# Kernel optimization log

Measured on AMD Instinct MI355X. Metric: run time of the kernel, lower is better.

## Reference

```python
import jax, jax.numpy as jnp
import numpy as np

N, E, F, H, C, L, B = 10000, 160000, 128, 8, 64, 8, 64
D = H * C  # 512 = hidden_dim * num_heads
BN_EPS = 1e-5


def setup_inputs() -> dict:
    key = jax.random.key(0)
    ks = jax.random.split(key, 24)

    def w(k, fi, fo, *lead):
        return jax.random.normal(k, (*lead, fi, fo), jnp.float32) / np.sqrt(fi).astype(np.float32)

    inp = {
        "x": jax.random.normal(ks[0], (N, F), jnp.float32),
        "edge_index": jax.random.randint(ks[1], (2, E), 0, N, jnp.int32),
        "batch": jnp.sort(jax.random.randint(ks[2], (N,), 0, B, jnp.int32)),
        # layer 0 projections (F -> D)
        "W0_q": w(ks[3], F, D), "b0_q": jnp.zeros((D,), jnp.float32),
        "W0_k": w(ks[4], F, D), "b0_k": jnp.zeros((D,), jnp.float32),
        "W0_v": w(ks[5], F, D), "b0_v": jnp.zeros((D,), jnp.float32),
        "W0_s": w(ks[6], F, D), "b0_s": jnp.zeros((D,), jnp.float32),
        # layers 1..7 projections (D -> D), stacked
        "Wq": w(ks[7], D, D, L - 1), "bq": jnp.zeros((L - 1, D), jnp.float32),
        "Wk": w(ks[8], D, D, L - 1), "bk": jnp.zeros((L - 1, D), jnp.float32),
        "Wv": w(ks[9], D, D, L - 1), "bv": jnp.zeros((L - 1, D), jnp.float32),
        "Ws": w(ks[10], D, D, L - 1), "bs": jnp.zeros((L - 1, D), jnp.float32),
        # BatchNorm affine params per layer
        "gamma": jnp.ones((L, D), jnp.float32),
        "beta": jnp.zeros((L, D), jnp.float32),
    }
    return inp


def _layer(x, src, dst, Wq, bq, Wk, bk, Wv, bv, Ws, bs, g, b):
    # TransformerConv (concat=True, root_weight=True, beta=False), eval dropout
    n = x.shape[0]
    q = (x @ Wq + bq).reshape(n, H, C)
    k = (x @ Wk + bk).reshape(n, H, C)
    v = (x @ Wv + bv).reshape(n, H, C)
    # per-edge attention logits [E, H]
    a = jnp.einsum('ehc,ehc->eh', q[dst], k[src]) / np.float32(np.sqrt(C))
    # softmax over incoming edges of each destination node
    amax = jax.ops.segment_max(a, dst, num_segments=n)
    a = jnp.exp(a - amax[dst])
    denom = jax.ops.segment_sum(a, dst, num_segments=n)
    a = a / (denom[dst] + 1e-16)
    msg = v[src] * a[:, :, None]                      # [E, H, C]
    out = jax.ops.segment_sum(msg, dst, num_segments=n).reshape(n, D)
    out = out + x @ Ws + bs                           # root/skip connection
    # BatchNorm1d (batch statistics) + ReLU
    mu = out.mean(axis=0)
    var = out.var(axis=0)
    out = (out - mu) / jnp.sqrt(var + BN_EPS) * g + b
    return jax.nn.relu(out)


def reference(x, edge_index, batch, W0_q, b0_q, W0_k, b0_k, W0_v, b0_v, W0_s, b0_s,
              Wq, bq, Wk, bk, Wv, bv, Ws, bs, gamma, beta):
    src, dst = edge_index[0], edge_index[1]
    counts = jnp.maximum(
        jax.ops.segment_sum(jnp.ones((N,), jnp.float32), batch, num_segments=B), 1.0)

    def pool(h):  # global_mean_pool
        return jax.ops.segment_sum(h, batch, num_segments=B) / counts[:, None]

    pooled = []
    h = _layer(x, src, dst, W0_q, b0_q, W0_k, b0_k, W0_v, b0_v, W0_s, b0_s,
               gamma[0], beta[0])
    pooled.append(pool(h))
    for i in range(L - 1):
        h = _layer(h, src, dst, Wq[i], bq[i], Wk[i], bk[i], Wv[i], bv[i],
                   Ws[i], bs[i], gamma[i + 1], beta[i + 1])
        pooled.append(pool(h))
    return jnp.concatenate(pooled, axis=1)  # [B, L*D]
```

## Files before the change

kernel.cpp:

```cpp
#include <hip/hip_runtime.h>

#define NN 10000
#define EE 160000
#define FF 128
#define LL 8
#define BB 64
#define DD 512
#define ND (NN * DD)

typedef unsigned short u16;
typedef __attribute__((ext_vector_type(8))) short short8;
typedef __attribute__((ext_vector_type(8))) _Float16 f16x8;
typedef __attribute__((ext_vector_type(4))) float f32x4;
typedef __attribute__((ext_vector_type(4))) u16 u16x4;

__device__ __forceinline__ u16 f2h(float f) {
  return __builtin_bit_cast(u16, (_Float16)f);
}
__device__ __forceinline__ float h2f(u16 h) {
  return (float)__builtin_bit_cast(_Float16, h);
}

#define GLOAD_LDS16(gp, lp)                                                   \
  __builtin_amdgcn_global_load_lds(                                           \
      (const __attribute__((address_space(1))) void*)(gp),                    \
      (__attribute__((address_space(3))) void*)(lp), 16, 0, 0)

__global__ void k_toh(const float* __restrict__ in, u16* __restrict__ out, int n4) {
  int i = blockIdx.x * 256 + threadIdx.x;
  if (i >= n4) return;
  float4 v = ((const float4*)in)[i];
  u16x4 h;
  h.x = f2h(v.x); h.y = f2h(v.y); h.z = f2h(v.z); h.w = f2h(v.w);
  ((u16x4*)out)[i] = h;
}

__global__ void k_convw(const float* __restrict__ W0, const float* __restrict__ W1,
                        const float* __restrict__ W2, const float* __restrict__ W3,
                        int K, u16* __restrict__ out) {
  __shared__ float t[32][33];
  int z = blockIdx.z;
  int lay = z >> 2, mat = z & 3;
  const float* W = ((mat == 0) ? W0 : (mat == 1) ? W1 : (mat == 2) ? W2 : W3) +
                   (size_t)lay * K * 512;
  int n0 = blockIdx.x * 32, k0 = blockIdx.y * 32;
  int tx = threadIdx.x, ty = threadIdx.y;
#pragma unroll
  for (int i = 0; i < 4; ++i)
    t[ty + 8 * i][tx] = W[(size_t)(k0 + ty + 8 * i) * 512 + n0 + tx];
  __syncthreads();
#pragma unroll
  for (int i = 0; i < 4; ++i) {
    int n = n0 + ty + 8 * i;
    float val = t[tx][ty + 8 * i];
    size_t o = ((size_t)lay * 2048 + mat * 512 + n) * K + k0 + tx;
    out[o] = f2h(val);
  }
}

__global__ void k_fbias(const float* __restrict__ b0q, const float* __restrict__ b0k,
                        const float* __restrict__ b0v, const float* __restrict__ b0s,
                        const float* __restrict__ bq, const float* __restrict__ bk,
                        const float* __restrict__ bv, const float* __restrict__ bs,
                        float* __restrict__ biasf) {
  int j = blockIdx.x * 256 + threadIdx.x;
  int l = j >> 11, m = (j >> 9) & 3, c = j & 511;
  const float* p;
  if (l == 0) {
    p = (m == 0) ? b0q : (m == 1) ? b0k : (m == 2) ? b0v : b0s;
  } else {
    const float* base = (m == 0) ? bq : (m == 1) ? bk : (m == 2) ? bv : bs;
    p = base + (size_t)(l - 1) * 512;
  }
  biasf[j] = p[c];
}

__global__ __launch_bounds__(256) void k_gemm(
    const u16* __restrict__ Ag, const u16* __restrict__ Bg,
    const float* __restrict__ biasf,
    u16* __restrict__ oq16, u16* __restrict__ ok16, u16* __restrict__ ov16,
    float* __restrict__ os, int M, int K) {
  __shared__ short8 sA[2][512], sB[2][512];
  const int tid = threadIdx.x;
  const int jt = blockIdx.x, mt = blockIdx.y;
  const int m0 = mt * 128;
  const int mat = jt >> 2;
  const int nbase = (jt & 3) * 128;
  const int K8 = K >> 3;
  const int l = tid & 63;
  const int wr = tid >> 7, wc = (tid >> 6) & 1;
  const int g = l >> 4, li = l & 15;

  const int c0 = tid, c1 = tid + 256;
  const int r0 = c0 >> 2, r1 = c1 >> 2;
  const int j0 = (c0 & 3) ^ (r0 & 3) ^ ((r0 >> 2) & 3);
  const int j1 = (c1 & 3) ^ (r1 & 3) ^ ((r1 >> 2) & 3);
  const int am0 = min(m0 + r0, M - 1), am1 = min(m0 + r1, M - 1);
  const int brow = mat * 512 + nbase;
  const short8* gA = (const short8*)Ag;
  const short8* gB = (const short8*)Bg;
  const size_t a0 = (size_t)am0 * K8 + j0, a1 = (size_t)am1 * K8 + j1;
  const size_t b0 = (size_t)(brow + r0) * K8 + j0, b1 = (size_t)(brow + r1) * K8 + j1;

  const f32x4 zero4 = {0.f, 0.f, 0.f, 0.f};
  f32x4 acc[4][4];
#pragma unroll
  for (int i = 0; i < 4; ++i)
#pragma unroll
    for (int j = 0; j < 4; ++j) acc[i][j] = zero4;

  auto stage = [&](int buf, int kg) {
    GLOAD_LDS16(gA + a0 + kg, &sA[buf][c0]);
    GLOAD_LDS16(gA + a1 + kg, &sA[buf][c1]);
    GLOAD_LDS16(gB + b0 + kg, &sB[buf][c0]);
    GLOAD_LDS16(gB + b1 + kg, &sB[buf][c1]);
  };

  auto compute = [&](int buf) {
    f16x8 fa[4], fb[4];
#pragma unroll
    for (int mi = 0; mi < 4; ++mi) {
      int row = wr * 64 + mi * 16 + li;
      int idx = row * 4 + (g ^ (row & 3) ^ ((row >> 2) & 3));
      fa[mi] = __builtin_bit_cast(f16x8, sA[buf][idx]);
    }
#pragma unroll
    for (int ni = 0; ni < 4; ++ni) {
      int row = wc * 64 + ni * 16 + li;
      int idx = row * 4 + (g ^ (row & 3) ^ ((row >> 2) & 3));
      fb[ni] = __builtin_bit_cast(f16x8, sB[buf][idx]);
    }
#pragma unroll
    for (int mi = 0; mi < 4; ++mi)
#pragma unroll
      for (int ni = 0; ni < 4; ++ni)
        acc[mi][ni] = __builtin_amdgcn_mfma_f32_16x16x32_f16(fa[mi], fb[ni], acc[mi][ni], 0, 0, 0);
  };

  int buf = 0;
  stage(0, 0);
  __syncthreads();
  for (int kg = 4; kg < K8; kg += 4) {
    stage(buf ^ 1, kg);
    compute(buf);
    __syncthreads();
    buf ^= 1;
  }
  compute(buf);

#pragma unroll
  for (int mi = 0; mi < 4; ++mi) {
    int rbase = m0 + wr * 64 + mi * 16 + g * 4;
#pragma unroll
    for (int ni = 0; ni < 4; ++ni) {
      int col = nbase + wc * 64 + ni * 16 + li;
      float bv = biasf[(jt << 7) + wc * 64 + ni * 16 + li];
#pragma unroll
      for (int r = 0; r < 4; ++r) {
        int gm = rbase + r;
        if (gm < M) {
          float val = acc[mi][ni][r] + bv;
          size_t o = (size_t)gm * 512 + col;
          if (mat == 0) oq16[o] = f2h(val);
          else if (mat == 1) ok16[o] = f2h(val);
          else if (mat == 2) ov16[o] = f2h(val);
          else os[o] = val;
        }
      }
    }
  }
}

__global__ void k_count(const int* __restrict__ dst, int* __restrict__ counts) {
  int e = blockIdx.x * 256 + threadIdx.x;
  if (e < EE) atomicAdd(&counts[dst[e]], 1);
}

__global__ void k_scan(const int* __restrict__ counts, int* __restrict__ offs) {
  __shared__ int ws[1024];
  int t = threadIdx.x;
  int base = t * 10;
  int loc[10];
  int run = 0;
#pragma unroll
  for (int j = 0; j < 10; ++j) {
    int i = base + j;
    int v = (i < NN) ? counts[i] : 0;
    run += v;
    loc[j] = run;
  }
  ws[t] = run;
  __syncthreads();
  for (int d = 1; d < 1024; d <<= 1) {
    int x = (t >= d) ? ws[t - d] : 0;
    __syncthreads();
    ws[t] += x;
    __syncthreads();
  }
  int pre = (t > 0) ? ws[t - 1] : 0;
#pragma unroll
  for (int j = 0; j < 10; ++j) {
    int i = base + j;
    if (i < NN) offs[i + 1] = pre + loc[j];
  }
  if (t == 0) offs[0] = 0;
}

__global__ void k_scatter(const int* __restrict__ src, const int* __restrict__ dst,
                          const int* __restrict__ offs, int* __restrict__ cursor,
                          int* __restrict__ esrc) {
  int e = blockIdx.x * 256 + threadIdx.x;
  if (e < EE) {
    int d = dst[e];
    int pos = offs[d] + atomicAdd(&cursor[d], 1);
    esrc[pos] = src[e];
  }
}

__global__ void k_bstart(const int* __restrict__ batch, int* __restrict__ bstart) {
  int n = blockIdx.x * 256 + threadIdx.x;
  if (n > NN) return;
  if (n == 0) {
    for (int b = 0; b <= batch[0]; ++b) bstart[b] = 0;
  } else if (n == NN) {
    for (int b = batch[NN - 1] + 1; b <= BB; ++b) bstart[b] = NN;
  } else {
    int bp = batch[n - 1], bn = batch[n];
    for (int b = bp + 1; b <= bn; ++b) bstart[b] = n;
  }
}

__device__ __forceinline__ void h8tof(short8 x, float* f) {
  f16x8 h = __builtin_bit_cast(f16x8, x);
#pragma unroll
  for (int j = 0; j < 8; ++j) f[j] = (float)h[j];
}

__global__ __launch_bounds__(256) void k_attn(
    const u16* __restrict__ q16, const u16* __restrict__ k16,
    const u16* __restrict__ v16, float* __restrict__ s,
    const int* __restrict__ offs, const int* __restrict__ esrc) {
  int node = blockIdx.x * 4 + (threadIdx.x >> 6);
  int l = threadIdx.x & 63;
  const short8* qp = (const short8*)q16;
  float qf[8];
  h8tof(qp[(size_t)node * 64 + l], qf);
  const short8* kp = (const short8*)k16;
  const short8* vp = (const short8*)v16;
  float m = -3.4e38f, ssum = 0.f;
  float a[8] = {0.f, 0.f, 0.f, 0.f, 0.f, 0.f, 0.f, 0.f};
  int e0 = offs[node], e1 = offs[node + 1];
  int e = e0;
  for (; e + 2 <= e1; e += 2) {
    int sn0 = esrc[e], sn1 = esrc[e + 1];
    short8 kk0 = kp[(size_t)sn0 * 64 + l];
    short8 kk1 = kp[(size_t)sn1 * 64 + l];
    short8 vv0 = vp[(size_t)sn0 * 64 + l];
    short8 vv1 = vp[(size_t)sn1 * 64 + l];
    float kf0[8], kf1[8];
    h8tof(kk0, kf0);
    h8tof(kk1, kf1);
    float d0 = 0.f, d1 = 0.f;
#pragma unroll
    for (int j = 0; j < 8; ++j) { d0 += qf[j] * kf0[j]; d1 += qf[j] * kf1[j]; }
    d0 += __shfl_xor(d0, 1); d1 += __shfl_xor(d1, 1);
    d0 += __shfl_xor(d0, 2); d1 += __shfl_xor(d1, 2);
    d0 += __shfl_xor(d0, 4); d1 += __shfl_xor(d1, 4);
    float vf0[8], vf1[8];
    h8tof(vv0, vf0);
    h8tof(vv1, vf1);
    {
      float logit = d0 * 0.125f;
      float mn = fmaxf(m, logit);
      float sc = __expf(m - mn), p = __expf(logit - mn);
      ssum = ssum * sc + p;
#pragma unroll
      for (int j = 0; j < 8; ++j) a[j] = a[j] * sc + p * vf0[j];
      m = mn;
    }
    {
      float logit = d1 * 0.125f;
      float mn = fmaxf(m, logit);
      float sc = __expf(m - mn), p = __expf(logit - mn);
      ssum = ssum * sc + p;
#pragma unroll
      for (int j = 0; j < 8; ++j) a[j] = a[j] * sc + p * vf1[j];
      m = mn;
    }
  }
  if (e < e1) {
    int sn0 = esrc[e];
    short8 kk0 = kp[(size_t)sn0 * 64 + l];
    short8 vv0 = vp[(size_t)sn0 * 64 + l];
    float kf0[8], vf0[8];
    h8tof(kk0, kf0);
    h8tof(vv0, vf0);
    float d0 = 0.f;
#pragma unroll
    for (int j = 0; j < 8; ++j) d0 += qf[j] * kf0[j];
    d0 += __shfl_xor(d0, 1);
    d0 += __shfl_xor(d0, 2);
    d0 += __shfl_xor(d0, 4);
    float logit = d0 * 0.125f;
    float mn = fmaxf(m, logit);
    float sc = __expf(m - mn), p = __expf(logit - mn);
    ssum = ssum * sc + p;
#pragma unroll
    for (int j = 0; j < 8; ++j) a[j] = a[j] * sc + p * vf0[j];
    m = mn;
  }
  float inv = (e1 > e0) ? 1.f / (ssum + 1e-16f) : 0.f;
  float4* sp = (float4*)(s + (size_t)node * 512);
  float4 s0 = sp[l * 2], s1 = sp[l * 2 + 1];
  s0.x += a[0] * inv; s0.y += a[1] * inv; s0.z += a[2] * inv; s0.w += a[3] * inv;
  s1.x += a[4] * inv; s1.y += a[5] * inv; s1.z += a[6] * inv; s1.w += a[7] * inv;
  sp[l * 2] = s0;
  sp[l * 2 + 1] = s1;
}

__global__ void k_bnstat(const float* __restrict__ s, float* __restrict__ bnpart) {
  int c = blockIdx.x * 256 + threadIdx.x;
  float sum = 0.f, sq = 0.f;
  for (int r = blockIdx.y; r < NN; r += 64) {
    float x = s[(size_t)r * 512 + c];
    sum += x;
    sq += x * x;
  }
  bnpart[blockIdx.y * 1024 + c] = sum;
  bnpart[blockIdx.y * 1024 + 512 + c] = sq;
}

__global__ void k_bnfinal(const float* __restrict__ bnpart, const float* __restrict__ gamma,
                          const float* __restrict__ beta, float* __restrict__ scale,
                          float* __restrict__ shift) {
  int c = threadIdx.x;
  float sum = 0.f, sq = 0.f;
  for (int j = 0; j < 64; ++j) {
    sum += bnpart[j * 1024 + c];
    sq += bnpart[j * 1024 + 512 + c];
  }
  float mu = sum * (1.f / NN);
  float var = sq * (1.f / NN) - mu * mu;
  float inv = rsqrtf(var + 1e-5f);
  float scl = gamma[c] * inv;
  scale[c] = scl;
  shift[c] = beta[c] - mu * scl;
}

__global__ void k_bnapply(const float* __restrict__ s, const float* __restrict__ scale,
                          const float* __restrict__ shift, u16* __restrict__ hh) {
  int i = blockIdx.x * 256 + threadIdx.x;
  float4 val = ((const float4*)s)[i];
  int c4 = i & 127;
  float4 scl = ((const float4*)scale)[c4];
  float4 shf = ((const float4*)shift)[c4];
  float4 r;
  r.x = fmaxf(val.x * scl.x + shf.x, 0.f);
  r.y = fmaxf(val.y * scl.y + shf.y, 0.f);
  r.z = fmaxf(val.z * scl.z + shf.z, 0.f);
  r.w = fmaxf(val.w * scl.w + shf.w, 0.f);
  u16x4 h;
  h.x = f2h(r.x); h.y = f2h(r.y); h.z = f2h(r.z); h.w = f2h(r.w);
  ((u16x4*)hh)[i] = h;
}

__global__ void k_pool(const u16* __restrict__ hh, const int* __restrict__ bstart,
                       float* __restrict__ out, int layer) {
  int c = blockIdx.x * 256 + threadIdx.x;
  int b = blockIdx.y;
  int r0 = bstart[b], r1 = bstart[b + 1];
  float sum = 0.f;
  for (int r = r0; r < r1; ++r) sum += h2f(hh[(size_t)r * 512 + c]);
  out[b * 4096 + layer * 512 + c] = sum / fmaxf((float)(r1 - r0), 1.f);
}

extern "C" void kernel_launch(void* const* d_in, const int* in_sizes, int n_in,
                              void* d_out, int out_size, void* d_ws, size_t ws_size,
                              hipStream_t stream) {
  (void)in_sizes; (void)n_in; (void)out_size; (void)ws_size;
  const float* x = (const float*)d_in[0];
  const int* ei = (const int*)d_in[1];
  const int* src = ei;
  const int* dst = ei + EE;
  const int* batch = (const int*)d_in[2];
  const float* W0q = (const float*)d_in[3];
  const float* b0q = (const float*)d_in[4];
  const float* W0k = (const float*)d_in[5];
  const float* b0k = (const float*)d_in[6];
  const float* W0v = (const float*)d_in[7];
  const float* b0v = (const float*)d_in[8];
  const float* W0s = (const float*)d_in[9];
  const float* b0s = (const float*)d_in[10];
  const float* Wq = (const float*)d_in[11];
  const float* bq = (const float*)d_in[12];
  const float* Wk = (const float*)d_in[13];
  const float* bk = (const float*)d_in[14];
  const float* Wv = (const float*)d_in[15];
  const float* bv = (const float*)d_in[16];
  const float* Ws = (const float*)d_in[17];
  const float* bs = (const float*)d_in[18];
  const float* gamma = (const float*)d_in[19];
  const float* beta = (const float*)d_in[20];
  float* out = (float*)d_out;

  char* w = (char*)d_ws;
  size_t off = 0;
  auto alloc = [&](size_t bytes) -> void* {
    void* p = w + off;
    off = (off + bytes + 255) & ~(size_t)255;
    return p;
  };
  u16* xh = (u16*)alloc((size_t)NN * FF * 2);
  u16* hh = (u16*)alloc((size_t)ND * 2);
  u16* qb16 = (u16*)alloc((size_t)ND * 2);
  u16* kb16 = (u16*)alloc((size_t)ND * 2);
  u16* vb16 = (u16*)alloc((size_t)ND * 2);
  float* sb = (float*)alloc((size_t)ND * 4);
  u16* wt0 = (u16*)alloc((size_t)4 * 512 * FF * 2);
  u16* wtN = (u16*)alloc((size_t)7 * 4 * 512 * 512 * 2);
  float* biasf = (float*)alloc((size_t)LL * 2048 * 4);
  float* bnpart = (float*)alloc((size_t)64 * 1024 * 4);
  float* bnscale = (float*)alloc(512 * 4);
  float* bnshift = (float*)alloc(512 * 4);
  int* counts = (int*)alloc(NN * 4);
  int* offs = (int*)alloc((NN + 1) * 4);
  int* cursor = (int*)alloc(NN * 4);
  int* esrc = (int*)alloc(EE * 4);
  int* bstart = (int*)alloc((BB + 1) * 4);

  hipMemsetAsync(counts, 0, NN * 4, stream);
  hipMemsetAsync(cursor, 0, NN * 4, stream);
  k_count<<<EE / 256, 256, 0, stream>>>(dst, counts);
  k_scan<<<1, 1024, 0, stream>>>(counts, offs);
  k_scatter<<<EE / 256, 256, 0, stream>>>(src, dst, offs, cursor, esrc);
  k_bstart<<<(NN + 256) / 256, 256, 0, stream>>>(batch, bstart);
  k_toh<<<(NN * FF / 4) / 256, 256, 0, stream>>>(x, xh, NN * FF / 4);
  k_convw<<<dim3(16, FF / 32, 4), dim3(32, 8), 0, stream>>>(W0q, W0k, W0v, W0s, FF, wt0);
  k_convw<<<dim3(16, 16, 28), dim3(32, 8), 0, stream>>>(Wq, Wk, Wv, Ws, DD, wtN);
  k_fbias<<<64, 256, 0, stream>>>(b0q, b0k, b0v, b0s, bq, bk, bv, bs, biasf);

  for (int layer = 0; layer < LL; ++layer) {
    int K = (layer == 0) ? FF : DD;
    const u16* A = (layer == 0) ? xh : hh;
    const u16* Bm = (layer == 0) ? wt0 : wtN + (size_t)(layer - 1) * 2048 * 512;
    k_gemm<<<dim3(16, 79), 256, 0, stream>>>(A, Bm, biasf + layer * 2048,
                                             qb16, kb16, vb16, sb, NN, K);
    k_attn<<<NN / 4, 256, 0, stream>>>(qb16, kb16, vb16, sb, offs, esrc);
    k_bnstat<<<dim3(2, 64), 256, 0, stream>>>(sb, bnpart);
    k_bnfinal<<<1, 512, 0, stream>>>(bnpart, gamma + layer * DD, beta + layer * DD,
                                     bnscale, bnshift);
    k_bnapply<<<(ND / 4) / 256, 256, 0, stream>>>(sb, bnscale, bnshift, hh);
    k_pool<<<dim3(2, 64), 256, 0, stream>>>(hh, bstart, out, layer);
  }
}
```

Measured before the change: 1.726 ms.

## Store skip/output buffer in fp16, unroll attention by four, fuse BN finalize into apply

The root-connection output and the attention result are now stored in fp16 rather than fp32, which halves the traffic through the GEMM epilogue, the attention read-modify-write, the BN statistics pass and the BN apply pass. The attention edge loop is unrolled to four edges so more gathers are in flight at once. BN statistics now use vectorized 8-wide loads with a shared-memory reduction, and the separate finalize kernel is folded into the apply kernel, which drops one launch per layer. The cost is lower precision on the pre-BN activations and a redundant recomputation of scale and shift in every apply block.

```diff
diff --git a/kernel.cpp b/kernel.cpp
--- a/kernel.cpp
+++ b/kernel.cpp
@@ -19,6 +19,11 @@
 }
 __device__ __forceinline__ float h2f(u16 h) {
   return (float)__builtin_bit_cast(_Float16, h);
+}
+__device__ __forceinline__ void h8tof(short8 x, float* f) {
+  f16x8 h = __builtin_bit_cast(f16x8, x);
+#pragma unroll
+  for (int j = 0; j < 8; ++j) f[j] = (float)h[j];
 }
 
 #define GLOAD_LDS16(gp, lp)                                                   \
@@ -79,7 +84,7 @@
     const u16* __restrict__ Ag, const u16* __restrict__ Bg,
     const float* __restrict__ biasf,
     u16* __restrict__ oq16, u16* __restrict__ ok16, u16* __restrict__ ov16,
-    float* __restrict__ os, int M, int K) {
+    u16* __restrict__ os16, int M, int K) {
   __shared__ short8 sA[2][512], sB[2][512];
   const int tid = threadIdx.x;
   const int jt = blockIdx.x, mt = blockIdx.y;
@@ -148,6 +153,7 @@
   }
   compute(buf);
 
+  u16* outp = (mat == 0) ? oq16 : (mat == 1) ? ok16 : (mat == 2) ? ov16 : os16;
 #pragma unroll
   for (int mi = 0; mi < 4; ++mi) {
     int rbase = m0 + wr * 64 + mi * 16 + g * 4;
@@ -158,14 +164,7 @@
 #pragma unroll
       for (int r = 0; r < 4; ++r) {
         int gm = rbase + r;
-        if (gm < M) {
-          float val = acc[mi][ni][r] + bv;
-          size_t o = (size_t)gm * 512 + col;
-          if (mat == 0) oq16[o] = f2h(val);
-          else if (mat == 1) ok16[o] = f2h(val);
-          else if (mat == 2) ov16[o] = f2h(val);
-          else os[o] = val;
-        }
+        if (gm < M) outp[(size_t)gm * 512 + col] = f2h(acc[mi][ni][r] + bv);
       }
     }
   }
@@ -230,15 +229,9 @@
   }
 }
 
-__device__ __forceinline__ void h8tof(short8 x, float* f) {
-  f16x8 h = __builtin_bit_cast(f16x8, x);
-#pragma unroll
-  for (int j = 0; j < 8; ++j) f[j] = (float)h[j];
-}
-
 __global__ __launch_bounds__(256) void k_attn(
     const u16* __restrict__ q16, const u16* __restrict__ k16,
-    const u16* __restrict__ v16, float* __restrict__ s,
+    const u16* __restrict__ v16, u16* __restrict__ s16,
     const int* __restrict__ offs, const int* __restrict__ esrc) {
   int node = blockIdx.x * 4 + (threadIdx.x >> 6);
   int l = threadIdx.x & 63;
@@ -251,24 +244,32 @@
   float a[8] = {0.f, 0.f, 0.f, 0.f, 0.f, 0.f, 0.f, 0.f};
   int e0 = offs[node], e1 = offs[node + 1];
   int e = e0;
-  for (; e + 2 <= e1; e += 2) {
-    int sn0 = esrc[e], sn1 = esrc[e + 1];
+  for (; e + 4 <= e1; e += 4) {
+    int sn0 = esrc[e], sn1 = esrc[e + 1], sn2 = esrc[e + 2], sn3 = esrc[e + 3];
     short8 kk0 = kp[(size_t)sn0 * 64 + l];
     short8 kk1 = kp[(size_t)sn1 * 64 + l];
+    short8 kk2 = kp[(size_t)sn2 * 64 + l];
+    short8 kk3 = kp[(size_t)sn3 * 64 + l];
     short8 vv0 = vp[(size_t)sn0 * 64 + l];
     short8 vv1 = vp[(size_t)sn1 * 64 + l];
-    float kf0[8], kf1[8];
-    h8tof(kk0, kf0);
-    h8tof(kk1, kf1);
-    float d0 = 0.f, d1 = 0.f;
-#pragma unroll
-    for (int j = 0; j < 8; ++j) { d0 += qf[j] * kf0[j]; d1 += qf[j] * kf1[j]; }
+    short8 vv2 = vp[(size_t)sn2 * 64 + l];
+    short8 vv3 = vp[(size_t)sn3 * 64 + l];
+    float kf0[8], kf1[8], kf2[8], kf3[8];
+    h8tof(kk0, kf0); h8tof(kk1, kf1); h8tof(kk2, kf2); h8tof(kk3, kf3);
+    float d0 = 0.f, d1 = 0.f, d2 = 0.f, d3 = 0.f;
+#pragma unroll
+    for (int j = 0; j < 8; ++j) {
+      d0 += qf[j] * kf0[j]; d1 += qf[j] * kf1[j];
+      d2 += qf[j] * kf2[j]; d3 += qf[j] * kf3[j];
+    }
     d0 += __shfl_xor(d0, 1); d1 += __shfl_xor(d1, 1);
+    d2 += __shfl_xor(d2, 1); d3 += __shfl_xor(d3, 1);
     d0 += __shfl_xor(d0, 2); d1 += __shfl_xor(d1, 2);
+    d2 += __shfl_xor(d2, 2); d3 += __shfl_xor(d3, 2);
     d0 += __shfl_xor(d0, 4); d1 += __shfl_xor(d1, 4);
-    float vf0[8], vf1[8];
-    h8tof(vv0, vf0);
-    h8tof(vv1, vf1);
+    d2 += __shfl_xor(d2, 4); d3 += __shfl_xor(d3, 4);
+    float vf0[8], vf1[8], vf2[8], vf3[8];
+    h8tof(vv0, vf0); h8tof(vv1, vf1); h8tof(vv2, vf2); h8tof(vv3, vf3);
     {
       float logit = d0 * 0.125f;
       float mn = fmaxf(m, logit);
@@ -287,8 +288,26 @@
       for (int j = 0; j < 8; ++j) a[j] = a[j] * sc + p * vf1[j];
       m = mn;
     }
-  }
-  if (e < e1) {
+    {
+      float logit = d2 * 0.125f;
+      float mn = fmaxf(m, logit);
+      float sc = __expf(m - mn), p = __expf(logit - mn);
+      ssum = ssum * sc + p;
+#pragma unroll
+      for (int j = 0; j < 8; ++j) a[j] = a[j] * sc + p * vf2[j];
+      m = mn;
+    }
+    {
+      float logit = d3 * 0.125f;
+      float mn = fmaxf(m, logit);
+      float sc = __expf(m - mn), p = __expf(logit - mn);
+      ssum = ssum * sc + p;
+#pragma unroll
+      for (int j = 0; j < 8; ++j) a[j] = a[j] * sc + p * vf3[j];
+      m = mn;
+    }
+  }
+  for (; e < e1; ++e) {
     int sn0 = esrc[e];
     short8 kk0 = kp[(size_t)sn0 * 64 + l];
     short8 vv0 = vp[(size_t)sn0 * 64 + l];
@@ -310,58 +329,87 @@
     m = mn;
   }
   float inv = (e1 > e0) ? 1.f / (ssum + 1e-16f) : 0.f;
-  float4* sp = (float4*)(s + (size_t)node * 512);
-  float4 s0 = sp[l * 2], s1 = sp[l * 2 + 1];
-  s0.x += a[0] * inv; s0.y += a[1] * inv; s0.z += a[2] * inv; s0.w += a[3] * inv;
-  s1.x += a[4] * inv; s1.y += a[5] * inv; s1.z += a[6] * inv; s1.w += a[7] * inv;
-  sp[l * 2] = s0;
-  sp[l * 2 + 1] = s1;
-}
-
-__global__ void k_bnstat(const float* __restrict__ s, float* __restrict__ bnpart) {
-  int c = blockIdx.x * 256 + threadIdx.x;
-  float sum = 0.f, sq = 0.f;
-  for (int r = blockIdx.y; r < NN; r += 64) {
-    float x = s[(size_t)r * 512 + c];
-    sum += x;
-    sq += x * x;
-  }
-  bnpart[blockIdx.y * 1024 + c] = sum;
-  bnpart[blockIdx.y * 1024 + 512 + c] = sq;
-}
-
-__global__ void k_bnfinal(const float* __restrict__ bnpart, const float* __restrict__ gamma,
-                          const float* __restrict__ beta, float* __restrict__ scale,
-                          float* __restrict__ shift) {
-  int c = threadIdx.x;
-  float sum = 0.f, sq = 0.f;
-  for (int j = 0; j < 64; ++j) {
-    sum += bnpart[j * 1024 + c];
-    sq += bnpart[j * 1024 + 512 + c];
-  }
-  float mu = sum * (1.f / NN);
-  float var = sq * (1.f / NN) - mu * mu;
-  float inv = rsqrtf(var + 1e-5f);
-  float scl = gamma[c] * inv;
-  scale[c] = scl;
-  shift[c] = beta[c] - mu * scl;
-}
-
-__global__ void k_bnapply(const float* __restrict__ s, const float* __restrict__ scale,
-                          const float* __restrict__ shift, u16* __restrict__ hh) {
-  int i = blockIdx.x * 256 + threadIdx.x;
-  float4 val = ((const float4*)s)[i];
-  int c4 = i & 127;
-  float4 scl = ((const float4*)scale)[c4];
-  float4 shf = ((const float4*)shift)[c4];
-  float4 r;
-  r.x = fmaxf(val.x * scl.x + shf.x, 0.f);
-  r.y = fmaxf(val.y * scl.y + shf.y, 0.f);
-  r.z = fmaxf(val.z * scl.z + shf.z, 0.f);
-  r.w = fmaxf(val.w * scl.w + shf.w, 0.f);
-  u16x4 h;
-  h.x = f2h(r.x); h.y = f2h(r.y); h.z = f2h(r.z); h.w = f2h(r.w);
-  ((u16x4*)hh)[i] = h;
+  short8* sp = (short8*)s16;
+  short8 srow = sp[(size_t)node * 64 + l];
+  float sf[8];
+  h8tof(srow, sf);
+  short8 hout;
+#pragma unroll
+  for (int j = 0; j < 8; ++j) hout[j] = (short)f2h(sf[j] + a[j] * inv);
+  sp[(size_t)node * 64 + l] = hout;
+}
+
+__global__ __launch_bounds__(256) void k_bnstat(const u16* __restrict__ s16,
+                                                float* __restrict__ bnpart) {
+  __shared__ float red[256][8];
+  int tid = threadIdx.x, blk = blockIdx.x;
+  int g = tid & 63;
+  int w = blk * 4 + (tid >> 6);
+  float sum[8] = {0, 0, 0, 0, 0, 0, 0, 0};
+  float sq[8] = {0, 0, 0, 0, 0, 0, 0, 0};
+  const short8* sp = (const short8*)s16;
+  for (int r = w; r < NN; r += 256) {
+    float f[8];
+    h8tof(sp[(size_t)r * 64 + g], f);
+#pragma unroll
+    for (int j = 0; j < 8; ++j) { sum[j] += f[j]; sq[j] += f[j] * f[j]; }
+  }
+#pragma unroll
+  for (int j = 0; j < 8; ++j) red[tid][j] = sum[j];
+  __syncthreads();
+  if (tid < 64) {
+#pragma unroll
+    for (int j = 0; j < 8; ++j) {
+      float t = red[tid][j] + red[tid + 64][j] + red[tid + 128][j] + red[tid + 192][j];
+      bnpart[blk * 1024 + tid * 8 + j] = t;
+    }
+  }
+  __syncthreads();
+#pragma unroll
+  for (int j = 0; j < 8; ++j) red[tid][j] = sq[j];
+  __syncthreads();
+  if (tid < 64) {
+#pragma unroll
+    for (int j = 0; j < 8; ++j) {
+      float t = red[tid][j] + red[tid + 64][j] + red[tid + 128][j] + red[tid + 192][j];
+      bnpart[blk * 1024 + 512 + tid * 8 + j] = t;
+    }
+  }
+}
+
+__global__ __launch_bounds__(256) void k_bnapply(
+    const u16* __restrict__ s16, const float* __restrict__ bnpart,
+    const float* __restrict__ gamma, const float* __restrict__ beta,
+    u16* __restrict__ hh) {
+  __shared__ float ssc[1024];
+  int tid = threadIdx.x;
+  for (int c = tid; c < 512; c += 256) {
+    float sum = 0.f, sq = 0.f;
+    for (int p = 0; p < 64; ++p) {
+      sum += bnpart[p * 1024 + c];
+      sq += bnpart[p * 1024 + 512 + c];
+    }
+    float mu = sum * (1.f / NN);
+    float var = sq * (1.f / NN) - mu * mu;
+    float inv = rsqrtf(var + 1e-5f);
+    float scl = gamma[c] * inv;
+    ssc[c] = scl;
+    ssc[512 + c] = beta[c] - mu * scl;
+  }
+  __syncthreads();
+  const short8* sp = (const short8*)s16;
+  short8* hp = (short8*)hh;
+  int total = gridDim.x * 256;
+  for (int j = blockIdx.x * 256 + tid; j < ND / 8; j += total) {
+    int c0 = (j & 63) * 8;
+    float f[8];
+    h8tof(sp[j], f);
+    short8 h;
+#pragma unroll
+    for (int jj = 0; jj < 8; ++jj)
+      h[jj] = (short)f2h(fmaxf(f[jj] * ssc[c0 + jj] + ssc[512 + c0 + jj], 0.f));
+    hp[j] = h;
+  }
 }
 
 __global__ void k_pool(const u16* __restrict__ hh, const int* __restrict__ bstart,
@@ -371,7 +419,7 @@
   int r0 = bstart[b], r1 = bstart[b + 1];
   float sum = 0.f;
   for (int r = r0; r < r1; ++r) sum += h2f(hh[(size_t)r * 512 + c]);
-  out[b * 4096 + layer * 512 + c] = sum / fmaxf((float)(r1 - r0), 1.f);
+  out[(size_t)b * 4096 + layer * 512 + c] = sum / fmaxf((float)(r1 - r0), 1.f);
 }
 
 extern "C" void kernel_launch(void* const* d_in, const int* in_sizes, int n_in,
@@ -415,13 +463,11 @@
   u16* qb16 = (u16*)alloc((size_t)ND * 2);
   u16* kb16 = (u16*)alloc((size_t)ND * 2);
   u16* vb16 = (u16*)alloc((size_t)ND * 2);
-  float* sb = (float*)alloc((size_t)ND * 4);
+  u16* sb16 = (u16*)alloc((size_t)ND * 2);
   u16* wt0 = (u16*)alloc((size_t)4 * 512 * FF * 2);
   u16* wtN = (u16*)alloc((size_t)7 * 4 * 512 * 512 * 2);
   float* biasf = (float*)alloc((size_t)LL * 2048 * 4);
   float* bnpart = (float*)alloc((size_t)64 * 1024 * 4);
-  float* bnscale = (float*)alloc(512 * 4);
-  float* bnshift = (float*)alloc(512 * 4);
   int* counts = (int*)alloc(NN * 4);
   int* offs = (int*)alloc((NN + 1) * 4);
   int* cursor = (int*)alloc(NN * 4);
@@ -444,12 +490,11 @@
     const u16* A = (layer == 0) ? xh : hh;
     const u16* Bm = (layer == 0) ? wt0 : wtN + (size_t)(layer - 1) * 2048 * 512;
     k_gemm<<<dim3(16, 79), 256, 0, stream>>>(A, Bm, biasf + layer * 2048,
-                                             qb16, kb16, vb16, sb, NN, K);
-    k_attn<<<NN / 4, 256, 0, stream>>>(qb16, kb16, vb16, sb, offs, esrc);
-    k_bnstat<<<dim3(2, 64), 256, 0, stream>>>(sb, bnpart);
-    k_bnfinal<<<1, 512, 0, stream>>>(bnpart, gamma + layer * DD, beta + layer * DD,
-                                     bnscale, bnshift);
-    k_bnapply<<<(ND / 4) / 256, 256, 0, stream>>>(sb, bnscale, bnshift, hh);
+                                             qb16, kb16, vb16, sb16, NN, K);
+    k_attn<<<NN / 4, 256, 0, stream>>>(qb16, kb16, vb16, sb16, offs, esrc);
+    k_bnstat<<<64, 256, 0, stream>>>(sb16, bnpart);
+    k_bnapply<<<320, 256, 0, stream>>>(sb16, bnpart, gamma + layer * DD,
+                                       beta + layer * DD, hh);
     k_pool<<<dim3(2, 64), 256, 0, stream>>>(hh, bstart, out, layer);
   }
 }
```

Result: faster. 1.386 ms (-19.7%).
